# Performance work log

Measured on AMD Instinct MI355X. Metric: run time of the kernel, lower is better.

Reference implementation:

```python
import jax, jax.numpy as jnp
import numpy as np

B, N, T, F_IN = 4, 1024, 16, 32
H1, H2 = 128, 128
LH = H2 // 2          # LSTM hidden = 64
MLP_H = H2 // 4       # 32
NEG = -9e15
ALPHA = 0.2           # LeakyReLU slope


def _xavier(k, shape):
    lim = float(np.sqrt(6.0 / (shape[0] + shape[1])))
    return jax.random.uniform(k, shape, jnp.float32, -lim, lim)


def _unif(k, shape, s):
    return jax.random.uniform(k, shape, jnp.float32, -s, s)


def setup_inputs() -> dict:
    key = jax.random.key(0)
    ks = jax.random.split(key, 16)
    x = jax.random.normal(ks[0], (B, N, T, F_IN), dtype=jnp.float32)
    adj = jax.random.randint(ks[1], (B, N, N), 0, 2, dtype=jnp.int32)
    # GAT layer 1 & 2
    W1 = _xavier(ks[2], (F_IN, H1)); a1 = _xavier(ks[3], (2 * H1, 1))
    W2 = _xavier(ks[4], (H1, H2));   a2 = _xavier(ks[5], (2 * H2, 1))
    # LSTM (torch gate order i,f,g,o)
    s = 1.0 / np.sqrt(LH)
    W_ih = _unif(ks[6], (4 * LH, H2), s)
    W_hh = _unif(ks[7], (4 * LH, LH), s)
    b_ih = _unif(ks[8], (4 * LH,), s)
    b_hh = _unif(ks[9], (4 * LH,), s)
    # Output MLP: 64 -> 32 -> 1
    s1 = 1.0 / np.sqrt(LH)
    Wo1 = _unif(ks[10], (LH, MLP_H), s1); bo1 = _unif(ks[11], (MLP_H,), s1)
    s2 = 1.0 / np.sqrt(MLP_H)
    Wo2 = _unif(ks[12], (MLP_H, 1), s2);  bo2 = _unif(ks[13], (1,), s2)
    return {"x": x, "adj": adj, "W1": W1, "a1": a1, "W2": W2, "a2": a2,
            "W_ih": W_ih, "W_hh": W_hh, "b_ih": b_ih, "b_hh": b_hh,
            "Wo1": Wo1, "bo1": bo1, "Wo2": Wo2, "bo2": bo2}


def _gat(h, mask, W, a):
    # h: (B,N,Fin) -> (B,N,Fout). Decompose cat([Wh_i,Wh_j]) @ a into two rank-1 scores.
    Wh = h @ W                             # (B,N,Fout)
    Fo = W.shape[1]
    s_src = Wh @ a[:Fo, 0]                 # (B,N)
    s_dst = Wh @ a[Fo:, 0]                 # (B,N)
    e = jax.nn.leaky_relu(s_src[:, :, None] + s_dst[:, None, :], ALPHA)  # (B,N,N)
    att = jnp.where(mask, e, NEG)
    att = jax.nn.softmax(att, axis=-1)
    return jax.nn.elu(att @ Wh)            # GAT layer's own ELU (concat=True)


def reference(x, adj, W1, a1, W2, a2, W_ih, W_hh, b_ih, b_hh, Wo1, bo1, Wo2, bo2):
    mask = adj > 0                         # (B,N,N)

    def per_t(ht):                         # ht: (B,N,F_IN)
        h = jax.nn.elu(_gat(ht, mask, W1, a1))   # outer F.elu as in GNNModel.forward
        h = jax.nn.elu(_gat(h, mask, W2, a2))
        return h

    g = jax.vmap(per_t, in_axes=2, out_axes=2)(x)   # (B,N,T,H2)
    seq = g.reshape(B * N, T, H2)

    def step(carry, xt):
        h, c = carry
        gates = xt @ W_ih.T + b_ih + h @ W_hh.T + b_hh
        i, f, gg, o = jnp.split(gates, 4, axis=-1)
        c = jax.nn.sigmoid(f) * c + jax.nn.sigmoid(i) * jnp.tanh(gg)
        h = jax.nn.sigmoid(o) * jnp.tanh(c)
        return (h, c), None

    init = (jnp.zeros((B * N, LH), x.dtype), jnp.zeros((B * N, LH), x.dtype))
    (hT, _), _ = jax.lax.scan(step, init, jnp.swapaxes(seq, 0, 1))  # scan over T

    out = jax.nn.relu(hT @ Wo1 + bo1) @ Wo2 + bo2   # (B*N, 1)
    return out.reshape(B, N, 1)
```

## Files before the change

kernel.cpp:

```cpp
#include <hip/hip_runtime.h>
#include <hip/hip_bf16.h>
#include <math.h>

#define BB 4
#define NN 1024
#define TT 16
#define FIN 32
#define HH 128
#define LH 64
#define MLPH 32

typedef __attribute__((ext_vector_type(8))) short short8;
typedef __attribute__((ext_vector_type(4))) float f32x4;
typedef unsigned short u16;
typedef unsigned int u32;

union AFu { u32 u[4]; short8 s; };

__device__ __forceinline__ u16 f2b(float f) {
    union { float f; u32 u; } v; v.f = f;
    u32 u = v.u;
    return (u16)((u + 0x7FFFu + ((u >> 16) & 1u)) >> 16);
}
__device__ __forceinline__ float b2f(u16 h) {
    union { u32 u; float f; } v; v.u = ((u32)h) << 16;
    return v.f;
}
__device__ __forceinline__ float frcp(float x) {
    float r; asm("v_rcp_f32 %0, %1" : "=v"(r) : "v"(x)); return r;
}
__device__ __forceinline__ float fsig(float x) {
    return frcp(1.f + __expf(-x));
}
__device__ __forceinline__ float ftanh(float x) {
    return __builtin_fmaf(2.f, frcp(1.f + __expf(-2.f * x)), -1.f);
}
__device__ __forceinline__ void gload_lds16(const void* g, void* l) {
    __builtin_amdgcn_global_load_lds((const __attribute__((address_space(1))) unsigned int*)g,
                                     (__attribute__((address_space(3))) unsigned int*)l, 16, 0, 0);
}

__global__ __launch_bounds__(256) void k_pre(const float* __restrict__ W1, const float* __restrict__ W2,
                      const float* __restrict__ W_ih, const float* __restrict__ W_hh,
                      const float* __restrict__ b_ih, const float* __restrict__ b_hh,
                      u16* W1T, u16* W2T, u16* WihB, u16* WhhB, float* bsum) {
    int gi = blockIdx.x * 256 + threadIdx.x;
    for (int i = gi; i < 128 * 32; i += 16384) { int c = i >> 5, k = i & 31; W1T[i] = f2b(W1[k * 128 + c]); }
    for (int i = gi; i < 128 * 128; i += 16384) { int c = i >> 7, k = i & 127; W2T[i] = f2b(W2[k * 128 + c]); }
    for (int i = gi; i < 256 * 128; i += 16384) WihB[i] = f2b(W_ih[i]);
    for (int i = gi; i < 256 * 64; i += 16384) WhhB[i] = f2b(W_hh[i]);
    if (gi < 256) bsum[gi] = b_ih[gi] + b_hh[gi];
}

__global__ __launch_bounds__(256) void k_mask(const int* __restrict__ adj, unsigned long long* __restrict__ bm) {
    int gw = (blockIdx.x * 256 + threadIdx.x) >> 6;
    int lane = threadIdx.x & 63;
    for (int u = gw; u < (BB * NN * NN) / 64; u += 1024) {
        unsigned long long m = __ballot(adj[(size_t)u * 64 + lane] > 0);
        if (lane == 0) bm[u] = m;
    }
}


__global__ __launch_bounds__(256) void k_projA(const float* __restrict__ x, const u16* __restrict__ W1T,
                                               const float* __restrict__ a1,
                                               u16* __restrict__ WhT, float* __restrict__ ssrc,
                                               float* __restrict__ sdst) {
    __shared__ float tile[64][132];
    __shared__ float sA[256];
    int bt = blockIdx.x >> 4, i0 = (blockIdx.x & 15) << 6;
    int b = bt >> 4, t = bt & 15;
    int tid = threadIdx.x, w = tid >> 6, l = tid & 63;
    int lr = l & 15, lg = l >> 4;
    sA[tid] = a1[tid];
    int i = i0 + 16 * w + lr;
    const float* xp = x + ((size_t)((b << 10) + i) * TT + t) * FIN + 8 * lg;
    float4 x0 = *(const float4*)xp;
    float4 x1 = *(const float4*)(xp + 4);
    short8 af;
    af[0] = (short)f2b(x0.x); af[1] = (short)f2b(x0.y); af[2] = (short)f2b(x0.z); af[3] = (short)f2b(x0.w);
    af[4] = (short)f2b(x1.x); af[5] = (short)f2b(x1.y); af[6] = (short)f2b(x1.z); af[7] = (short)f2b(x1.w);
    f32x4 zz = {0.f, 0.f, 0.f, 0.f};
#pragma unroll
    for (int tc = 0; tc < 8; ++tc) {
        short8 bf = *(const short8*)(W1T + ((16 * tc + lr) << 5) + 8 * lg);
        f32x4 d = __builtin_amdgcn_mfma_f32_16x16x32_bf16(af, bf, zz, 0, 0, 0);
#pragma unroll
        for (int r = 0; r < 4; ++r) tile[16 * w + 4 * lg + r][16 * tc + lr] = d[r];
    }
    __syncthreads();
    if (tid < 128) {
        int r = tid & 63;
        const float* av = sA + ((tid < 64) ? 0 : 128);
        float s = 0.f;
#pragma unroll 4
        for (int c = 0; c < 128; ++c) s += tile[r][c] * av[c];
        ((tid < 64) ? ssrc : sdst)[(bt << 10) + i0 + r] = s;
    }
    {
        int c = tid & 127, hh2 = tid >> 7;
        u16 tmp[32];
#pragma unroll
        for (int j = 0; j < 32; ++j) tmp[j] = f2b(tile[32 * hh2 + j][c]);
        int tc = c >> 4, lr2 = c & 15;
        u16* dst = WhT + (size_t)bt * 131072 + (i0 >> 6) * 8192 + ((hh2 << 3) + tc) * 512 + lr2 * 8;
#pragma unroll
        for (int lg2 = 0; lg2 < 4; ++lg2) *(short8*)(dst + lg2 * 128) = *(const short8*)(tmp + 8 * lg2);
    }
}

__global__ __launch_bounds__(256) void k_projB(const u16* __restrict__ h1, const u16* __restrict__ W2T,
                                               const float* __restrict__ a2,
                                               u16* __restrict__ WhT, float* __restrict__ ssrc,
                                               float* __restrict__ sdst) {
    __shared__ float tile[64][132];
    __shared__ float sA[256];
    int bt = blockIdx.x >> 4, i0 = (blockIdx.x & 15) << 6;
    int tid = threadIdx.x, w = tid >> 6, l = tid & 63;
    int lr = l & 15, lg = l >> 4;
    sA[tid] = a2[tid];
    const u16* ap = h1 + (size_t)bt * 131072 + ((i0 >> 4) + w) * 2048 + l * 8;
    f32x4 acc[8];
#pragma unroll
    for (int tc = 0; tc < 8; ++tc) acc[tc] = (f32x4){0.f, 0.f, 0.f, 0.f};
#pragma unroll
    for (int ch = 0; ch < 4; ++ch) {
        short8 af = *(const short8*)(ap + ch * 512);
#pragma unroll
        for (int tc = 0; tc < 8; ++tc) {
            short8 bf = *(const short8*)(W2T + ((16 * tc + lr) << 7) + 32 * ch + 8 * lg);
            acc[tc] = __builtin_amdgcn_mfma_f32_16x16x32_bf16(af, bf, acc[tc], 0, 0, 0);
        }
    }
#pragma unroll
    for (int tc = 0; tc < 8; ++tc)
#pragma unroll
        for (int r = 0; r < 4; ++r) tile[16 * w + 4 * lg + r][16 * tc + lr] = acc[tc][r];
    __syncthreads();
    if (tid < 128) {
        int r = tid & 63;
        const float* av = sA + ((tid < 64) ? 0 : 128);
        float s = 0.f;
#pragma unroll 4
        for (int c = 0; c < 128; ++c) s += tile[r][c] * av[c];
        ((tid < 64) ? ssrc : sdst)[(bt << 10) + i0 + r] = s;
    }
    {
        int c = tid & 127, hh2 = tid >> 7;
        u16 tmp[32];
#pragma unroll
        for (int j = 0; j < 32; ++j) tmp[j] = f2b(tile[32 * hh2 + j][c]);
        int tc = c >> 4, lr2 = c & 15;
        u16* dst = WhT + (size_t)bt * 131072 + (i0 >> 6) * 8192 + ((hh2 << 3) + tc) * 512 + lr2 * 8;
#pragma unroll
        for (int lg2 = 0; lg2 < 4; ++lg2) *(short8*)(dst + lg2 * 128) = *(const short8*)(tmp + 8 * lg2);
    }
}

template <bool GX>
__global__ __launch_bounds__(256, 2) void k_attn(const u16* __restrict__ WhT, const float* __restrict__ ssrc,
                                                 const float* __restrict__ sdst, const u32* __restrict__ bm,
                                                 u16* __restrict__ hout, const u16* __restrict__ WihB,
                                                 const float* __restrict__ bsum, u16* __restrict__ Gx) {
    __shared__ __align__(16) u16 Bbuf[2][8192];
    __shared__ __align__(16) float Ej[1024];
    __shared__ __align__(16) float Fj[1024];
    __shared__ u32 bml[32 * 132];
    int bt = blockIdx.x >> 3, i0b = (blockIdx.x & 7) << 7;
    int b = bt >> 4;
    int tid = threadIdx.x, wv = tid >> 6, l = tid & 63;
    int lr = l & 15, lg = l >> 4;

    for (int k = tid; k < 1024; k += 256) {
        float sdv = sdst[(bt << 10) + k];
        Ej[k] = __expf(sdv);
        Fj[k] = __expf(0.2f * sdv);
    }
    for (int k = tid; k < 4096; k += 256) {
        int r = k >> 5, wd = k & 31;
        bml[wd * 132 + r] = bm[(((size_t)(b << 10) + i0b + r) << 5) + wd];
    }
    const u16* wbase = WhT + (size_t)bt * 131072;
    {
        int u0 = wv << 2;
#pragma unroll
        for (int p = 0; p < 4; ++p) {
            int u = u0 + p;
            gload_lds16(wbase + u * 512 + l * 8, Bbuf[0] + u * 512);
        }
    }
    int rb = i0b + (wv << 5);
    float si0 = ssrc[(bt << 10) + rb + lr];
    float si1 = ssrc[(bt << 10) + rb + 16 + lr];
    float Ei0 = __expf(si0), Fi0 = __expf(0.2f * si0);
    float Ei1 = __expf(si1), Fi1 = __expf(0.2f * si1);
    f32x4 acc[2][8];
#pragma unroll
    for (int rt = 0; rt < 2; ++rt)
#pragma unroll
        for (int tc = 0; tc < 8; ++tc) acc[rt][tc] = (f32x4){0.f, 0.f, 0.f, 0.f};
    f32x4 accd[2];
    accd[0] = (f32x4){0.f, 0.f, 0.f, 0.f};
    accd[1] = (f32x4){0.f, 0.f, 0.f, 0.f};
    short8 bone;
#pragma unroll
    for (int e = 0; e < 8; ++e) bone[e] = (short)0x3F80;
    int rl0 = (wv << 5) + lr;
    __syncthreads();

    for (int c = 0; c < 16; ++c) {
        int cur = c & 1;
        if (c < 15) {
            int u0 = wv << 2;
#pragma unroll
            for (int p = 0; p < 4; ++p) {
                int u = u0 + p;
                gload_lds16(wbase + (c + 1) * 8192 + u * 512 + l * 8, Bbuf[cur ^ 1] + u * 512);
            }
        }
#pragma unroll
        for (int jcl = 0; jcl < 2; ++jcl) {
            int jc = 2 * c + jcl;
            short8 bfr[8];
#pragma unroll
            for (int tc = 0; tc < 8; ++tc)
                bfr[tc] = *(const short8*)(Bbuf[cur] + ((((jcl << 3) + tc) << 6) + l) * 8);
            const float* ejp = Ej + (jc << 5) + (lg << 3);
            const float* fjp = Fj + (jc << 5) + (lg << 3);
            float4 e0 = *(const float4*)ejp, e1 = *(const float4*)(ejp + 4);
            float4 f0 = *(const float4*)fjp, f1 = *(const float4*)(fjp + 4);
            u32 w0 = bml[jc * 132 + rl0];
            u32 w1 = bml[jc * 132 + rl0 + 16];
            AFu af0, af1;
            {
                u32 byt = (w0 >> (lg << 3)) & 0xFFu;
                float pA[8] = {fmaxf(Ei0 * e0.x, Fi0 * f0.x), fmaxf(Ei0 * e0.y, Fi0 * f0.y),
                               fmaxf(Ei0 * e0.z, Fi0 * f0.z), fmaxf(Ei0 * e0.w, Fi0 * f0.w),
                               fmaxf(Ei0 * e1.x, Fi0 * f1.x), fmaxf(Ei0 * e1.y, Fi0 * f1.y),
                               fmaxf(Ei0 * e1.z, Fi0 * f1.z), fmaxf(Ei0 * e1.w, Fi0 * f1.w)};
#pragma unroll
                for (int q = 0; q < 4; ++q) {
                    u32 m0 = (u32)(-(int)((byt >> (2 * q)) & 1u));
                    u32 m1 = (u32)(-(int)((byt >> (2 * q + 1)) & 1u));
                    float p0 = __uint_as_float(__float_as_uint(pA[2 * q]) & m0);
                    float p1 = __uint_as_float(__float_as_uint(pA[2 * q + 1]) & m1);
                    asm("v_cvt_pk_bf16_f32 %0, %1, %2" : "=v"(af0.u[q]) : "v"(p0), "v"(p1));
                }
            }
            {
                u32 byt = (w1 >> (lg << 3)) & 0xFFu;
                float pA[8] = {fmaxf(Ei1 * e0.x, Fi1 * f0.x), fmaxf(Ei1 * e0.y, Fi1 * f0.y),
                               fmaxf(Ei1 * e0.z, Fi1 * f0.z), fmaxf(Ei1 * e0.w, Fi1 * f0.w),
                               fmaxf(Ei1 * e1.x, Fi1 * f1.x), fmaxf(Ei1 * e1.y, Fi1 * f1.y),
                               fmaxf(Ei1 * e1.z, Fi1 * f1.z), fmaxf(Ei1 * e1.w, Fi1 * f1.w)};
#pragma unroll
                for (int q = 0; q < 4; ++q) {
                    u32 m0 = (u32)(-(int)((byt >> (2 * q)) & 1u));
                    u32 m1 = (u32)(-(int)((byt >> (2 * q + 1)) & 1u));
                    float p0 = __uint_as_float(__float_as_uint(pA[2 * q]) & m0);
                    float p1 = __uint_as_float(__float_as_uint(pA[2 * q + 1]) & m1);
                    asm("v_cvt_pk_bf16_f32 %0, %1, %2" : "=v"(af1.u[q]) : "v"(p0), "v"(p1));
                }
            }
#pragma unroll
            for (int tc = 0; tc < 8; ++tc) {
                acc[0][tc] = __builtin_amdgcn_mfma_f32_16x16x32_bf16(af0.s, bfr[tc], acc[0][tc], 0, 0, 0);
                acc[1][tc] = __builtin_amdgcn_mfma_f32_16x16x32_bf16(af1.s, bfr[tc], acc[1][tc], 0, 0, 0);
            }
            accd[0] = __builtin_amdgcn_mfma_f32_16x16x32_bf16(af0.s, bone, accd[0], 0, 0, 0);
            accd[1] = __builtin_amdgcn_mfma_f32_16x16x32_bf16(af1.s, bone, accd[1], 0, 0, 0);
        }
        __syncthreads();
    }
    char* hb = (char*)(&Bbuf[0][0]) + (wv << 13);
#pragma unroll
    for (int rt = 0; rt < 2; ++rt) {
        float inv[4];
#pragma unroll
        for (int r = 0; r < 4; ++r) inv[r] = 1.f / accd[rt][r];
#pragma unroll
        for (int tc = 0; tc < 8; ++tc)
#pragma unroll
            for (int r = 0; r < 4; ++r) {
                float v = acc[rt][tc][r] * inv[r];
                v = v > 0.f ? v : (__expf(v) - 1.f);
                v = v > 0.f ? v : (__expf(v) - 1.f);
                int row = (rt << 4) + (lg << 2) + r;
                int col = (tc << 4) + lr;
                *(u16*)(hb + (row << 8) + ((col << 1) ^ ((row & 7) << 4))) = f2b(v);
            }
    }
    asm volatile("s_waitcnt lgkmcnt(0)" ::: "memory");
    __builtin_amdgcn_sched_barrier(0);

    if (!GX) {
        int rtile0 = rb >> 4;
        u16* dstb = hout + (size_t)bt * 131072;
#pragma unroll
        for (int rt = 0; rt < 2; ++rt)
#pragma unroll
            for (int ch = 0; ch < 4; ++ch) {
                int row = (rt << 4) + lr;
                int colb = (ch << 5) + (lg << 3);
                short8 v = *(const short8*)(hb + (row << 8) + ((colb << 1) ^ ((row & 7) << 4)));
                *(short8*)(dstb + (size_t)(rtile0 + rt) * 2048 + ch * 512 + l * 8) = v;
            }
    } else {
        int t = bt & 15;
#pragma unroll
        for (int rt = 0; rt < 2; ++rt) {
            f32x4 accg[16];
#pragma unroll
            for (int tc = 0; tc < 16; ++tc) accg[tc] = (f32x4){0.f, 0.f, 0.f, 0.f};
#pragma unroll
            for (int ch = 0; ch < 4; ++ch) {
                int row = (rt << 4) + lr;
                short8 af2 = *(const short8*)(hb + (row << 8) + (((ch << 6) + (lg << 4)) ^ ((lr & 7) << 4)));
#pragma unroll
                for (int tc = 0; tc < 16; ++tc) {
                    short8 bf = *(const short8*)(WihB + ((16 * tc + lr) << 7) + (ch << 5) + 8 * lg);
                    accg[tc] = __builtin_amdgcn_mfma_f32_16x16x32_bf16(af2, bf, accg[tc], 0, 0, 0);
                }
            }
            int node = i0b + (wv << 5) + (rt << 4);
            int grp = (b << 6) + (node >> 4);
            u16* gdst = Gx + (size_t)t * 1048576 + (size_t)grp * 4096 + l * 8;
#pragma unroll
            for (int q = 0; q < 8; ++q) {
                short8 v;
#pragma unroll
                for (int r = 0; r < 4; ++r) {
                    v[r]     = (short)f2b(accg[2 * q][r]     + bsum[((2 * q) << 4) + lr]);
                    v[4 + r] = (short)f2b(accg[2 * q + 1][r] + bsum[((2 * q + 1) << 4) + lr]);
                }
                *(short8*)(gdst + q * 512) = v;
            }
        }
    }
}

__global__ __launch_bounds__(64, 1) void k_lstm(const u16* __restrict__ Gx, const u16* __restrict__ WhhB,
                                                const float* __restrict__ Wo1, const float* __restrict__ bo1,
                                                const float* __restrict__ Wo2, const float* __restrict__ bo2,
                                                float* __restrict__ out) {
    __shared__ u16 hls[16 * 72];
    __shared__ float hf[16 * 65];
    __shared__ float wo1[64 * 32];
    __shared__ float wo2[32];
    int grp = blockIdx.x;
    int m0 = grp << 4;
    int l = threadIdx.x, lr = l & 15, lg = l >> 4;
    for (int k = l; k < 64 * 32; k += 64) wo1[k] = Wo1[k];
    if (l < 32) wo2[l] = Wo2[l];
    for (int k = l; k < 16 * 72; k += 64) hls[k] = 0;
    short8 bh[16][2];
#pragma unroll
    for (int tc = 0; tc < 16; ++tc)
#pragma unroll
        for (int ch = 0; ch < 2; ++ch)
            bh[tc][ch] = *(const short8*)(WhhB + ((16 * tc + lr) << 6) + 32 * ch + 8 * lg);
    float cst[4][4], hreg[4][4];
#pragma unroll
    for (int r = 0; r < 4; ++r)
#pragma unroll
        for (int q = 0; q < 4; ++q) cst[r][q] = 0.f;
    const u16* gp = Gx + ((size_t)grp << 12) + l * 8;
    short8 gx0[8], gx1[8];
#pragma unroll
    for (int q = 0; q < 8; ++q) gx0[q] = *(const short8*)(gp + q * 512);
    __syncthreads();
#pragma unroll
    for (int t = 0; t < TT; ++t) {
        if (t < 15) {
#pragma unroll
            for (int q = 0; q < 8; ++q) {
                short8 v = *(const short8*)(gp + (size_t)(t + 1) * 1048576 + q * 512);
                if (t & 1) gx0[q] = v; else gx1[q] = v;
            }
        }
        f32x4 acc[16];
#pragma unroll
        for (int q = 0; q < 8; ++q) {
            short8 v = (t & 1) ? gx1[q] : gx0[q];
#pragma unroll
            for (int r = 0; r < 4; ++r) {
                acc[2 * q][r]     = b2f((u16)v[r]);
                acc[2 * q + 1][r] = b2f((u16)v[4 + r]);
            }
        }
#pragma unroll
        for (int ch = 0; ch < 2; ++ch) {
            short8 af = *(const short8*)(hls + lr * 72 + 32 * ch + 8 * lg);
#pragma unroll
            for (int tc = 0; tc < 16; ++tc)
                acc[tc] = __builtin_amdgcn_mfma_f32_16x16x32_bf16(af, bh[tc][ch], acc[tc], 0, 0, 0);
        }
#pragma unroll
        for (int r = 0; r < 4; ++r)
#pragma unroll
            for (int q = 0; q < 4; ++q) {
                float iv = fsig(acc[q][r]);
                float fv = fsig(acc[q + 4][r]);
                float gv = ftanh(acc[q + 8][r]);
                float ov = fsig(acc[q + 12][r]);
                float cn = __builtin_fmaf(fv, cst[r][q], iv * gv);
                cst[r][q] = cn;
                hreg[r][q] = ov * ftanh(cn);
            }
        __syncthreads();
#pragma unroll
        for (int r = 0; r < 4; ++r)
#pragma unroll
            for (int q = 0; q < 4; ++q)
                hls[(4 * lg + r) * 72 + 16 * q + lr] = f2b(hreg[r][q]);
        __syncthreads();
    }
#pragma unroll
    for (int r = 0; r < 4; ++r)
#pragma unroll
        for (int q = 0; q < 4; ++q)
            hf[(4 * lg + r) * 65 + 16 * q + lr] = hreg[r][q];
    __syncthreads();
    {
        int r = l & 15, p = l >> 4;
        float hid[8];
#pragma unroll
        for (int q = 0; q < 8; ++q) hid[q] = bo1[8 * p + q];
        for (int j = 0; j < 64; ++j) {
            float hv = hf[r * 65 + j];
#pragma unroll
            for (int q = 0; q < 8; ++q) hid[q] += hv * wo1[j * 32 + 8 * p + q];
        }
        float po = 0.f;
#pragma unroll
        for (int q = 0; q < 8; ++q) po += fmaxf(hid[q], 0.f) * wo2[8 * p + q];
        po += __shfl_xor(po, 16);
        po += __shfl_xor(po, 32);
        if (p == 0) out[m0 + r] = po + bo2[0];
    }
}

extern "C" void kernel_launch(void* const* d_in, const int* in_sizes, int n_in,
                              void* d_out, int out_size, void* d_ws, size_t ws_size,
                              hipStream_t stream) {
    const float* x    = (const float*)d_in[0];
    const int*   adj  = (const int*)d_in[1];
    const float* W1   = (const float*)d_in[2];
    const float* a1   = (const float*)d_in[3];
    const float* W2   = (const float*)d_in[4];
    const float* a2   = (const float*)d_in[5];
    const float* W_ih = (const float*)d_in[6];
    const float* W_hh = (const float*)d_in[7];
    const float* b_ih = (const float*)d_in[8];
    const float* b_hh = (const float*)d_in[9];
    const float* Wo1  = (const float*)d_in[10];
    const float* bo1  = (const float*)d_in[11];
    const float* Wo2  = (const float*)d_in[12];
    const float* bo2  = (const float*)d_in[13];
    float* out = (float*)d_out;

    char* w = (char*)d_ws;
    const size_t SLOT = (size_t)8388608 * sizeof(u16);
    u16* A  = (u16*)w;
    u16* Bf = (u16*)(w + SLOT);
    u16* C  = (u16*)(w + 2 * SLOT);
    char* sm = w + 3 * SLOT;
    float* s1s = (float*)sm;
    float* s1d = s1s + 65536;
    float* s2s = s1d + 65536;
    float* s2d = s2s + 65536;
    u32* BM  = (u32*)(s2d + 65536);
    u16* W1T = (u16*)(BM + 131072);
    u16* W2T = W1T + 4096;
    u16* WihB = W2T + 16384;
    u16* WhhB = WihB + 32768;
    float* BS = (float*)(WhhB + 16384);
    u16* Gx = Bf;

    k_pre<<<64, 256, 0, stream>>>(W1, W2, W_ih, W_hh, b_ih, b_hh, W1T, W2T, WihB, WhhB, BS);
    k_mask<<<256, 256, 0, stream>>>(adj, (unsigned long long*)BM);
    k_projA<<<1024, 256, 0, stream>>>(x, W1T, a1, A, s1s, s1d);
    k_attn<false><<<512, 256, 0, stream>>>(A, s1s, s1d, BM, Bf, nullptr, nullptr, nullptr);
    k_projB<<<1024, 256, 0, stream>>>(Bf, W2T, a2, C, s2s, s2d);
    k_attn<true><<<512, 256, 0, stream>>>(C, s2s, s2d, BM, nullptr, WihB, BS, Gx);
    k_lstm<<<256, 64, 0, stream>>>(Gx, WhhB, Wo1, bo1, Wo2, bo2, out);
}
```

Baseline: 183.9 us.

## Deepen attention kernel B-tile prefetch to four-stage pipeline with finer chunks

The attention kernel's double-buffered 16KB B chunks (two j-chunks each) become four 8KB buffers of one j-chunk each, with three stages issued before the prologue exp and mask loads. Each stage is waited on with a counted vmcnt plus a raw barrier instead of a full __syncthreads, which is meant to hide global-to-LDS latency better and start loads earlier. The WhT layout written by both projection kernels is changed to match the 32-row chunking. The risk is more barriers per block and tighter reliance on hand-counted vmcnt values being correct.

```diff
diff --git a/kernel.cpp b/kernel.cpp
--- a/kernel.cpp
+++ b/kernel.cpp
@@ -103,7 +103,7 @@
 #pragma unroll
         for (int j = 0; j < 32; ++j) tmp[j] = f2b(tile[32 * hh2 + j][c]);
         int tc = c >> 4, lr2 = c & 15;
-        u16* dst = WhT + (size_t)bt * 131072 + (i0 >> 6) * 8192 + ((hh2 << 3) + tc) * 512 + lr2 * 8;
+        u16* dst = WhT + (size_t)bt * 131072 + ((i0 >> 5) + hh2) * 4096 + tc * 512 + lr2 * 8;
 #pragma unroll
         for (int lg2 = 0; lg2 < 4; ++lg2) *(short8*)(dst + lg2 * 128) = *(const short8*)(tmp + 8 * lg2);
     }
@@ -151,7 +151,7 @@
 #pragma unroll
         for (int j = 0; j < 32; ++j) tmp[j] = f2b(tile[32 * hh2 + j][c]);
         int tc = c >> 4, lr2 = c & 15;
-        u16* dst = WhT + (size_t)bt * 131072 + (i0 >> 6) * 8192 + ((hh2 << 3) + tc) * 512 + lr2 * 8;
+        u16* dst = WhT + (size_t)bt * 131072 + ((i0 >> 5) + hh2) * 4096 + tc * 512 + lr2 * 8;
 #pragma unroll
         for (int lg2 = 0; lg2 < 4; ++lg2) *(short8*)(dst + lg2 * 128) = *(const short8*)(tmp + 8 * lg2);
     }
@@ -162,7 +162,7 @@
                                                  const float* __restrict__ sdst, const u32* __restrict__ bm,
                                                  u16* __restrict__ hout, const u16* __restrict__ WihB,
                                                  const float* __restrict__ bsum, u16* __restrict__ Gx) {
-    __shared__ __align__(16) u16 Bbuf[2][8192];
+    __shared__ __align__(16) u16 Bbuf4[4][4096];
     __shared__ __align__(16) float Ej[1024];
     __shared__ __align__(16) float Fj[1024];
     __shared__ u32 bml[32 * 132];
@@ -170,6 +170,15 @@
     int b = bt >> 4;
     int tid = threadIdx.x, wv = tid >> 6, l = tid & 63;
     int lr = l & 15, lg = l >> 4;
+    const u16* wbase = WhT + (size_t)bt * 131072;
+
+#define STAGE(SC, BU)                                                               \
+    {                                                                               \
+        gload_lds16(wbase + (SC) * 4096 + (wv << 10) + l * 8,       &Bbuf4[BU][(wv << 10)]);       \
+        gload_lds16(wbase + (SC) * 4096 + (wv << 10) + 512 + l * 8, &Bbuf4[BU][(wv << 10) + 512]); \
+    }
+
+    STAGE(0, 0) STAGE(1, 1) STAGE(2, 2)
 
     for (int k = tid; k < 1024; k += 256) {
         float sdv = sdst[(bt << 10) + k];
@@ -179,15 +188,6 @@
     for (int k = tid; k < 4096; k += 256) {
         int r = k >> 5, wd = k & 31;
         bml[wd * 132 + r] = bm[(((size_t)(b << 10) + i0b + r) << 5) + wd];
-    }
-    const u16* wbase = WhT + (size_t)bt * 131072;
-    {
-        int u0 = wv << 2;
-#pragma unroll
-        for (int p = 0; p < 4; ++p) {
-            int u = u0 + p;
-            gload_lds16(wbase + u * 512 + l * 8, Bbuf[0] + u * 512);
-        }
     }
     int rb = i0b + (wv << 5);
     float si0 = ssrc[(bt << 10) + rb + lr];
@@ -208,71 +208,71 @@
     int rl0 = (wv << 5) + lr;
     __syncthreads();
 
-    for (int c = 0; c < 16; ++c) {
-        int cur = c & 1;
-        if (c < 15) {
-            int u0 = wv << 2;
-#pragma unroll
-            for (int p = 0; p < 4; ++p) {
-                int u = u0 + p;
-                gload_lds16(wbase + (c + 1) * 8192 + u * 512 + l * 8, Bbuf[cur ^ 1] + u * 512);
-            }
-        }
-#pragma unroll
-        for (int jcl = 0; jcl < 2; ++jcl) {
-            int jc = 2 * c + jcl;
-            short8 bfr[8];
-#pragma unroll
-            for (int tc = 0; tc < 8; ++tc)
-                bfr[tc] = *(const short8*)(Bbuf[cur] + ((((jcl << 3) + tc) << 6) + l) * 8);
-            const float* ejp = Ej + (jc << 5) + (lg << 3);
-            const float* fjp = Fj + (jc << 5) + (lg << 3);
-            float4 e0 = *(const float4*)ejp, e1 = *(const float4*)(ejp + 4);
-            float4 f0 = *(const float4*)fjp, f1 = *(const float4*)(fjp + 4);
-            u32 w0 = bml[jc * 132 + rl0];
-            u32 w1 = bml[jc * 132 + rl0 + 16];
-            AFu af0, af1;
-            {
-                u32 byt = (w0 >> (lg << 3)) & 0xFFu;
-                float pA[8] = {fmaxf(Ei0 * e0.x, Fi0 * f0.x), fmaxf(Ei0 * e0.y, Fi0 * f0.y),
-                               fmaxf(Ei0 * e0.z, Fi0 * f0.z), fmaxf(Ei0 * e0.w, Fi0 * f0.w),
-                               fmaxf(Ei0 * e1.x, Fi0 * f1.x), fmaxf(Ei0 * e1.y, Fi0 * f1.y),
-                               fmaxf(Ei0 * e1.z, Fi0 * f1.z), fmaxf(Ei0 * e1.w, Fi0 * f1.w)};
-#pragma unroll
-                for (int q = 0; q < 4; ++q) {
-                    u32 m0 = (u32)(-(int)((byt >> (2 * q)) & 1u));
-                    u32 m1 = (u32)(-(int)((byt >> (2 * q + 1)) & 1u));
-                    float p0 = __uint_as_float(__float_as_uint(pA[2 * q]) & m0);
-                    float p1 = __uint_as_float(__float_as_uint(pA[2 * q + 1]) & m1);
-                    asm("v_cvt_pk_bf16_f32 %0, %1, %2" : "=v"(af0.u[q]) : "v"(p0), "v"(p1));
-                }
-            }
-            {
-                u32 byt = (w1 >> (lg << 3)) & 0xFFu;
-                float pA[8] = {fmaxf(Ei1 * e0.x, Fi1 * f0.x), fmaxf(Ei1 * e0.y, Fi1 * f0.y),
-                               fmaxf(Ei1 * e0.z, Fi1 * f0.z), fmaxf(Ei1 * e0.w, Fi1 * f0.w),
-                               fmaxf(Ei1 * e1.x, Fi1 * f1.x), fmaxf(Ei1 * e1.y, Fi1 * f1.y),
-                               fmaxf(Ei1 * e1.z, Fi1 * f1.z), fmaxf(Ei1 * e1.w, Fi1 * f1.w)};
-#pragma unroll
-                for (int q = 0; q < 4; ++q) {
-                    u32 m0 = (u32)(-(int)((byt >> (2 * q)) & 1u));
-                    u32 m1 = (u32)(-(int)((byt >> (2 * q + 1)) & 1u));
-                    float p0 = __uint_as_float(__float_as_uint(pA[2 * q]) & m0);
-                    float p1 = __uint_as_float(__float_as_uint(pA[2 * q + 1]) & m1);
-                    asm("v_cvt_pk_bf16_f32 %0, %1, %2" : "=v"(af1.u[q]) : "v"(p0), "v"(p1));
-                }
-            }
-#pragma unroll
-            for (int tc = 0; tc < 8; ++tc) {
-                acc[0][tc] = __builtin_amdgcn_mfma_f32_16x16x32_bf16(af0.s, bfr[tc], acc[0][tc], 0, 0, 0);
-                acc[1][tc] = __builtin_amdgcn_mfma_f32_16x16x32_bf16(af1.s, bfr[tc], acc[1][tc], 0, 0, 0);
-            }
-            accd[0] = __builtin_amdgcn_mfma_f32_16x16x32_bf16(af0.s, bone, accd[0], 0, 0, 0);
-            accd[1] = __builtin_amdgcn_mfma_f32_16x16x32_bf16(af1.s, bone, accd[1], 0, 0, 0);
-        }
-        __syncthreads();
-    }
-    char* hb = (char*)(&Bbuf[0][0]) + (wv << 13);
+#define PHALF(AF, EI, FI, WW)                                                        \
+    {                                                                                \
+        u32 byt = ((WW) >> (lg << 3)) & 0xFFu;                                       \
+        float pA[8] = {fmaxf((EI) * e0.x, (FI) * f0.x), fmaxf((EI) * e0.y, (FI) * f0.y), \
+                       fmaxf((EI) * e0.z, (FI) * f0.z), fmaxf((EI) * e0.w, (FI) * f0.w), \
+                       fmaxf((EI) * e1.x, (FI) * f1.x), fmaxf((EI) * e1.y, (FI) * f1.y), \
+                       fmaxf((EI) * e1.z, (FI) * f1.z), fmaxf((EI) * e1.w, (FI) * f1.w)}; \
+        _Pragma("unroll")                                                            \
+        for (int q = 0; q < 4; ++q) {                                                \
+            u32 m0 = (u32)(-(int)((byt >> (2 * q)) & 1u));                           \
+            u32 m1 = (u32)(-(int)((byt >> (2 * q + 1)) & 1u));                       \
+            float p0 = __uint_as_float(__float_as_uint(pA[2 * q]) & m0);             \
+            float p1 = __uint_as_float(__float_as_uint(pA[2 * q + 1]) & m1);         \
+            asm("v_cvt_pk_bf16_f32 %0, %1, %2" : "=v"(AF.u[q]) : "v"(p0), "v"(p1));  \
+        }                                                                            \
+    }
+
+#define COMPUTE(JC, BU)                                                              \
+    {                                                                                \
+        short8 bfr[8];                                                               \
+        _Pragma("unroll")                                                            \
+        for (int tc = 0; tc < 8; ++tc)                                               \
+            bfr[tc] = *(const short8*)(&Bbuf4[BU][tc * 512 + l * 8]);                \
+        const float* ejp = Ej + ((JC) << 5) + (lg << 3);                             \
+        const float* fjp = Fj + ((JC) << 5) + (lg << 3);                             \
+        float4 e0 = *(const float4*)ejp, e1 = *(const float4*)(ejp + 4);             \
+        float4 f0 = *(const float4*)fjp, f1 = *(const float4*)(fjp + 4);             \
+        u32 w0 = bml[(JC) * 132 + rl0];                                              \
+        u32 w1 = bml[(JC) * 132 + rl0 + 16];                                         \
+        AFu af0, af1;                                                                \
+        PHALF(af0, Ei0, Fi0, w0)                                                     \
+        PHALF(af1, Ei1, Fi1, w1)                                                     \
+        _Pragma("unroll")                                                            \
+        for (int tc = 0; tc < 8; ++tc) {                                             \
+            acc[0][tc] = __builtin_amdgcn_mfma_f32_16x16x32_bf16(af0.s, bfr[tc], acc[0][tc], 0, 0, 0); \
+            acc[1][tc] = __builtin_amdgcn_mfma_f32_16x16x32_bf16(af1.s, bfr[tc], acc[1][tc], 0, 0, 0); \
+        }                                                                            \
+        accd[0] = __builtin_amdgcn_mfma_f32_16x16x32_bf16(af0.s, bone, accd[0], 0, 0, 0); \
+        accd[1] = __builtin_amdgcn_mfma_f32_16x16x32_bf16(af1.s, bone, accd[1], 0, 0, 0); \
+    }
+
+#define FENCE(VM)                                                                    \
+    asm volatile("s_waitcnt vmcnt(" VM ")" ::: "memory");                            \
+    __builtin_amdgcn_s_barrier();                                                    \
+    __builtin_amdgcn_sched_barrier(0);
+
+    for (int it = 0; it < 7; ++it) {
+        int c0 = it << 2;
+        STAGE(c0 + 3, 3) COMPUTE(c0 + 0, 0) FENCE("4")
+        STAGE(c0 + 4, 0) COMPUTE(c0 + 1, 1) FENCE("4")
+        STAGE(c0 + 5, 1) COMPUTE(c0 + 2, 2) FENCE("4")
+        STAGE(c0 + 6, 2) COMPUTE(c0 + 3, 3) FENCE("4")
+    }
+    STAGE(31, 3) COMPUTE(28, 0) FENCE("4")
+    COMPUTE(29, 1) FENCE("2")
+    COMPUTE(30, 2) FENCE("0")
+    COMPUTE(31, 3)
+    __syncthreads();
+
+#undef STAGE
+#undef PHALF
+#undef COMPUTE
+#undef FENCE
+
+    char* hb = (char*)(&Bbuf4[0][0]) + (wv << 13);
 #pragma unroll
     for (int rt = 0; rt < 2; ++rt) {
         float inv[4];
```

After: 189.5 us. 3.0% more time.
